# Performance work log

Measured on AMD Instinct MI355X. Metric: run time of the kernel, lower is better.

## Reference

```python
import jax, jax.numpy as jnp
import numpy as np

B, N, F, T, E, OUT = 16, 5000, 8, 12, 160000, 64


def setup_inputs() -> dict:
    key = jax.random.key(0)
    ks = jax.random.split(key, 20)
    d = {}
    d["x"] = jax.random.normal(ks[0], (B, N, F, T), dtype=jnp.float32)
    d["edge_index"] = jax.random.randint(ks[1], (2, E), 0, N, dtype=jnp.int32)
    def p(k, shape, scale=0.1):
        return jax.random.normal(k, shape, dtype=jnp.float32) * scale
    i = 2
    for g in ("z", "r", "h"):
        d[f"W{g}"] = p(ks[i], (F, OUT)); i += 1        # GCNConv weight
        d[f"b{g}"] = p(ks[i], (OUT,)); i += 1           # GCNConv bias
        d[f"L{g}"] = p(ks[i], (2 * OUT, OUT)); i += 1   # gate Linear weight
        d[f"lb{g}"] = p(ks[i], (OUT,)); i += 1          # gate Linear bias
    d["att"] = p(ks[i], (T,)); i += 1                   # A3TGCN attention logits
    d["fcW"] = p(ks[i], (OUT, T)); i += 1               # final Linear 64->periods
    d["fcb"] = p(ks[i], (T,))
    return d


def _gcn(xs, W, b, src, dst, norm, n_nodes):
    # xs: [M, N, F] -> D^{-1/2}(A+I)D^{-1/2} (xs W) + b
    support = xs @ W                                    # [M, N, OUT]
    msg = support[:, src, :] * norm[None, :, None]      # gather at source
    agg = jax.vmap(lambda m: jax.ops.segment_sum(m, dst, num_segments=n_nodes))(msg)
    return agg + b


def reference(x, edge_index, Wz, bz, Lz, lbz, Wr, br, Lr, lbr, Wh, bh, Lh, lbh, att, fcW, fcb):
    b_sz, n_nodes, _, periods = x.shape
    src, dst = edge_index[0], edge_index[1]
    loop = jnp.arange(n_nodes, dtype=src.dtype)
    src = jnp.concatenate([src, loop])                  # add self loops
    dst = jnp.concatenate([dst, loop])
    deg = jax.ops.segment_sum(jnp.ones(src.shape, jnp.float32), dst, num_segments=n_nodes)
    dinv = jnp.where(deg > 0, jax.lax.rsqrt(deg), 0.0)
    norm = dinv[src] * dinv[dst]                        # symmetric GCN normalization

    # In A3TGCN the hidden state is never carried across periods (stays zero),
    # so all periods are independent: fold T into the batch axis.
    xs = jnp.moveaxis(x, 3, 0).reshape(periods * b_sz, n_nodes, x.shape[2])
    H = jnp.zeros((periods * b_sz, n_nodes, Wz.shape[1]), x.dtype)

    Z = jax.nn.sigmoid(jnp.concatenate([_gcn(xs, Wz, bz, src, dst, norm, n_nodes), H], -1) @ Lz + lbz)
    R = jax.nn.sigmoid(jnp.concatenate([_gcn(xs, Wr, br, src, dst, norm, n_nodes), H], -1) @ Lr + lbr)
    Ht = jnp.tanh(jnp.concatenate([_gcn(xs, Wh, bh, src, dst, norm, n_nodes), H * R], -1) @ Lh + lbh)
    Hnew = Z * H + (1.0 - Z) * Ht                       # [T*B, N, 64]

    Hs = Hnew.reshape(periods, b_sz, n_nodes, -1)
    Hacc = jnp.einsum('t,tbnh->bnh', jax.nn.softmax(att), Hs)
    return Hacc @ fcW + fcb                             # [B, N, periods]
```

## Files before the change

kernel.cpp:

```cpp
#include <hip/hip_runtime.h>
#include <math.h>

#define BB 16
#define NN 5000
#define FF 8
#define TT 12
#define EE 160000
#define HH 64
#define EN (EE + NN)
#define XBSTRIDE 1920000
#define BSOFF    15360000


__global__ void k_count(const int* __restrict__ dst, int* __restrict__ deg) {
    int i = blockIdx.x * blockDim.x + threadIdx.x;
    if (i < EE) atomicAdd(&deg[dst[i]], 1);
}

__global__ __launch_bounds__(256) void k_scan_prep(
    const int* __restrict__ deg, int* __restrict__ offs, int* __restrict__ cursor,
    float* __restrict__ dinv,
    const float* __restrict__ Wz, const float* __restrict__ bz,
    const float* __restrict__ Lz, const float* __restrict__ lbz,
    const float* __restrict__ Wh, const float* __restrict__ bh,
    const float* __restrict__ Lh, const float* __restrict__ lbh,
    const float* __restrict__ att,
    float* __restrict__ G, float* __restrict__ C, float* __restrict__ sm) {
    int tid = threadIdx.x;
    if (blockIdx.x == 0) {
        __shared__ int s[256];
        int base = tid * 20;
        int cnt[20];
        int part = 0;
#pragma unroll
        for (int j = 0; j < 20; ++j) {
            int n = base + j;
            int c = (n < NN) ? deg[n] + 1 : 0;
            cnt[j] = c;
            part += c;
        }
        s[tid] = part;
        __syncthreads();
        for (int d = 1; d < 256; d <<= 1) {
            int v = (tid >= d) ? s[tid - d] : 0;
            __syncthreads();
            s[tid] += v;
            __syncthreads();
        }
        int run = s[tid] - part;
#pragma unroll
        for (int j = 0; j < 20; ++j) {
            int n = base + j;
            if (n < NN) {
                offs[n] = run;
                cursor[n] = run;
                dinv[n] = rsqrtf((float)cnt[j]);
                run += cnt[j];
            }
        }
        if (tid == 255) offs[NN] = s[255];
    } else {
        for (int idx = tid; idx < 1024; idx += 256) {
            int g = idx >> 9, rem = idx & 511, f = rem >> 6, o = rem & 63;
            const float* W = g ? Wh : Wz;
            const float* L = g ? Lh : Lz;
            float acc = 0.f;
            for (int k = 0; k < 64; ++k) acc += W[f * 64 + k] * L[k * 64 + o];
            G[idx] = acc;
        }
        for (int idx = tid; idx < 128; idx += 256) {
            int g = idx >> 6, o = idx & 63;
            const float* b = g ? bh : bz;
            const float* L = g ? Lh : Lz;
            const float* lb = g ? lbh : lbz;
            float acc = lb[o];
            for (int k = 0; k < 64; ++k) acc += b[k] * L[k * 64 + o];
            C[idx] = acc;
        }
        if (tid == 0) {
            float m = att[0];
            for (int t = 1; t < TT; ++t) m = fmaxf(m, att[t]);
            float e[TT], ss = 0.f;
            for (int t = 0; t < TT; ++t) { e[t] = __expf(att[t] - m); ss += e[t]; }
            for (int t = 0; t < TT; ++t) sm[t] = e[t] / ss;
        }
    }
}

__global__ void k_fill(const int* __restrict__ src, const int* __restrict__ dst,
                       int* cursor, const float* __restrict__ dinv,
                       int2* __restrict__ cedge) {
    int i = blockIdx.x * blockDim.x + threadIdx.x;
    if (i < EE) {
        int s = src[i], d = dst[i];
        int p = atomicAdd(&cursor[d], 1);
        cedge[p] = make_int2(s, __float_as_int(dinv[s] * dinv[d]));
    } else if (i < EN) {
        int n = i - EE;
        int p = atomicAdd(&cursor[n], 1);
        cedge[p] = make_int2(n, __float_as_int(dinv[n] * dinv[n]));
    } else if (i < EN + 8) {
        cedge[i] = make_int2(0, 0);
    }
}


#define EDGE(D)                                                         \
    {                                                                   \
        unsigned a_ = (unsigned)(D).x * 384u + voff;                    \
        float4 v_ = *(const float4*)(xbb + a_);                         \
        float w_ = __int_as_float((D).y);                               \
        acc.x += w_ * v_.x; acc.y += w_ * v_.y;                         \
        acc.z += w_ * v_.z; acc.w += w_ * v_.w;                         \
    }

__global__ __launch_bounds__(256) void k_fused(
    const float* __restrict__ x, const int* __restrict__ offs,
    const int2* __restrict__ cedge,
    const float* __restrict__ G, const float* __restrict__ C,
    const float* __restrict__ sm, const float* __restrict__ fcW,
    const float* __restrict__ fcb, float* __restrict__ out) {
    __shared__ __align__(16) float xals[4][2][96];
    __shared__ float hl[4][2][65];

    const int tid = threadIdx.x;
    const int wid = tid >> 6;
    const int lane = tid & 63;
    const int bp = blockIdx.x & 7;
    const int g = blockIdx.x >> 3;
    const int n = g * 4 + wid;

    int r0 = __builtin_amdgcn_readfirstlane(offs[n]);
    int r1 = __builtin_amdgcn_readfirstlane(offs[n + 1]);

    const char* xbb = (const char*)x + (size_t)bp * XBSTRIDE;

    if (lane < 48) {
        const unsigned voff = (unsigned)(lane / 24) * BSOFF + (unsigned)(lane % 24) * 16u;
        float4 acc = {0.f, 0.f, 0.f, 0.f};

        int k = r0;
        int2 p0 = cedge[k];
        int2 p1 = cedge[k + 1];
        int2 p2 = cedge[k + 2];
        int2 p3 = cedge[k + 3];
        while (k + 4 <= r1) {
            int2 d0 = p0, d1 = p1, d2 = p2, d3 = p3;
            k += 4;
            p0 = cedge[k];
            p1 = cedge[k + 1];
            p2 = cedge[k + 2];
            p3 = cedge[k + 3];
            EDGE(d0) EDGE(d1) EDGE(d2) EDGE(d3)
        }
        int rem = r1 - k;
        if (rem > 0) EDGE(p0)
        if (rem > 1) EDGE(p1)
        if (rem > 2) EDGE(p2)

        *(float4*)&xals[wid][lane / 24][(lane % 24) * 4] = acc;
    }
    __syncthreads();

    float gz[FF], gh[FF];
#pragma unroll
    for (int f = 0; f < FF; ++f) {
        gz[f] = G[f * 64 + lane];
        gh[f] = G[512 + f * 64 + lane];
    }
    float cz = C[lane], ch = C[64 + lane];
    float smv[TT];
#pragma unroll
    for (int t = 0; t < TT; ++t) smv[t] = sm[t];

#pragma unroll
    for (int bs = 0; bs < 2; ++bs) {
        float hacc = 0.f;
#pragma unroll
        for (int tq = 0; tq < 3; ++tq) {
            float4 xq[FF];
#pragma unroll
            for (int f = 0; f < FF; ++f)
                xq[f] = *(const float4*)&xals[wid][bs][f * TT + tq * 4];
#pragma unroll
            for (int tt = 0; tt < 4; ++tt) {
                float az = cz, ah = ch;
#pragma unroll
                for (int f = 0; f < FF; ++f) {
                    float v = ((const float*)&xq[f])[tt];
                    az += v * gz[f];
                    ah += v * gh[f];
                }
                float z = __builtin_amdgcn_rcpf(1.0f + __expf(-az));
                float th = 1.0f - 2.0f * __builtin_amdgcn_rcpf(__expf(2.0f * ah) + 1.0f);
                hacc += smv[tq * 4 + tt] * (1.0f - z) * th;
            }
        }
        hl[wid][bs][lane] = hacc;
    }
    __syncthreads();

    if (tid < 96) {
        int nw = tid / 24;
        int rem = tid % 24;
        int bs = rem / 12;
        int t = rem % 12;
        int nn2 = g * 4 + nw;
        int b = bp + bs * 8;
        float s = fcb[t];
#pragma unroll 16
        for (int o = 0; o < HH; ++o) s += hl[nw][bs][o] * fcW[o * TT + t];
        out[((size_t)b * NN + nn2) * TT + t] = s;
    }
}

extern "C" void kernel_launch(void* const* d_in, const int* in_sizes, int n_in,
                              void* d_out, int out_size, void* d_ws, size_t ws_size,
                              hipStream_t stream) {
    const float* x   = (const float*)d_in[0];
    const int*   ei  = (const int*)d_in[1];
    const float* Wz  = (const float*)d_in[2];
    const float* bz  = (const float*)d_in[3];
    const float* Lz  = (const float*)d_in[4];
    const float* lbz = (const float*)d_in[5];
    const float* Wh  = (const float*)d_in[10];
    const float* bh  = (const float*)d_in[11];
    const float* Lh  = (const float*)d_in[12];
    const float* lbh = (const float*)d_in[13];
    const float* att = (const float*)d_in[14];
    const float* fcW = (const float*)d_in[15];
    const float* fcb = (const float*)d_in[16];
    float* out = (float*)d_out;

    const int* src = ei;
    const int* dst = ei + EE;

    int2*  cedge  = (int2*)d_ws;
    int*   deg    = (int*)(cedge + EN + 8);
    int*   cursor = deg + NN;
    int*   offs   = cursor + NN;
    float* dinv   = (float*)(offs + NN + 1);
    float* G      = dinv + NN;
    float* C      = G + 1024;
    float* sm     = C + 128;

    hipMemsetAsync(deg, 0, NN * sizeof(int), stream);
    hipLaunchKernelGGL(k_count, dim3((EE + 255) / 256), dim3(256), 0, stream, dst, deg);
    hipLaunchKernelGGL(k_scan_prep, dim3(2), dim3(256), 0, stream,
                       deg, offs, cursor, dinv,
                       Wz, bz, Lz, lbz, Wh, bh, Lh, lbh, att, G, C, sm);
    hipLaunchKernelGGL(k_fill, dim3((EN + 8 + 255) / 256), dim3(256), 0, stream,
                       src, dst, cursor, dinv, cedge);
    hipLaunchKernelGGL(k_fused, dim3(1250 * 8), dim3(256), 0, stream,
                       x, offs, cedge, G, C, sm, fcW, fcb, out);
}
```

Baseline: 142.9 us.

## Pad CSR rows to multiples of 8 and vectorize gather, gates, and FC

Each node's CSR segment is padded to a multiple of 8 zero-weight entries, so the gather loop reads int4 edge pairs in blocks of 8 with no tail handling, at the cost of zeroing a larger workspace with memset. G, C and fcW are staged in LDS. Gate math uses exp2 with log2e folded into the precomputed weights, plus a combined sigmoid-tanh expression that needs a single reciprocal. The final linear layer writes two outputs per thread using packed float2 math. These changes cut the number of edge-load instructions, transcendental operations and global reads of the weights, while adding padding traffic and more LDS use.

```diff
diff --git a/kernel.cpp b/kernel.cpp
--- a/kernel.cpp
+++ b/kernel.cpp
@@ -1,15 +1,19 @@
 #include <hip/hip_runtime.h>
-#include <math.h>
-
-#define BB 16
+
 #define NN 5000
 #define FF 8
 #define TT 12
 #define EE 160000
 #define HH 64
 #define EN (EE + NN)
+#define CAP (EN + 7 * NN + 64)
 #define XBSTRIDE 1920000
 #define BSOFF    15360000
+
+typedef float f2  __attribute__((ext_vector_type(2)));
+typedef float f4v __attribute__((ext_vector_type(4)));
+
+#define LOG2E 1.44269504088896340736f
 
 
 __global__ void k_count(const int* __restrict__ dst, int* __restrict__ deg) {
@@ -30,14 +34,15 @@
     if (blockIdx.x == 0) {
         __shared__ int s[256];
         int base = tid * 20;
-        int cnt[20];
+        int pad[20], real[20];
         int part = 0;
 #pragma unroll
         for (int j = 0; j < 20; ++j) {
             int n = base + j;
             int c = (n < NN) ? deg[n] + 1 : 0;
-            cnt[j] = c;
-            part += c;
+            real[j] = c;
+            pad[j] = (c + 7) & ~7;
+            part += pad[j];
         }
         s[tid] = part;
         __syncthreads();
@@ -54,8 +59,8 @@
             if (n < NN) {
                 offs[n] = run;
                 cursor[n] = run;
-                dinv[n] = rsqrtf((float)cnt[j]);
-                run += cnt[j];
+                dinv[n] = rsqrtf((float)real[j]);
+                run += pad[j];
             }
         }
         if (tid == 255) offs[NN] = s[255];
@@ -66,7 +71,7 @@
             const float* L = g ? Lh : Lz;
             float acc = 0.f;
             for (int k = 0; k < 64; ++k) acc += W[f * 64 + k] * L[k * 64 + o];
-            G[idx] = acc;
+            G[idx] = acc * (g ? 2.0f * LOG2E : LOG2E);
         }
         for (int idx = tid; idx < 128; idx += 256) {
             int g = idx >> 6, o = idx & 63;
@@ -75,7 +80,7 @@
             const float* lb = g ? lbh : lbz;
             float acc = lb[o];
             for (int k = 0; k < 64; ++k) acc += b[k] * L[k * 64 + o];
-            C[idx] = acc;
+            C[idx] = acc * (g ? 2.0f * LOG2E : LOG2E);
         }
         if (tid == 0) {
             float m = att[0];
@@ -99,19 +104,18 @@
         int n = i - EE;
         int p = atomicAdd(&cursor[n], 1);
         cedge[p] = make_int2(n, __float_as_int(dinv[n] * dinv[n]));
-    } else if (i < EN + 8) {
-        cedge[i] = make_int2(0, 0);
-    }
-}
-
-
-#define EDGE(D)                                                         \
-    {                                                                   \
-        unsigned a_ = (unsigned)(D).x * 384u + voff;                    \
-        float4 v_ = *(const float4*)(xbb + a_);                         \
-        float w_ = __int_as_float((D).y);                               \
-        acc.x += w_ * v_.x; acc.y += w_ * v_.y;                         \
-        acc.z += w_ * v_.z; acc.w += w_ * v_.w;                         \
+    }
+}
+
+
+#define E2(Q)                                                     \
+    {                                                             \
+        unsigned a0_ = (unsigned)(Q).x * 384u + voff;             \
+        unsigned a1_ = (unsigned)(Q).z * 384u + voff;             \
+        f4v v0_ = *(const f4v*)(xbb + a0_);                       \
+        f4v v1_ = *(const f4v*)(xbb + a1_);                       \
+        acc += __int_as_float((Q).y) * v0_;                       \
+        acc += __int_as_float((Q).w) * v1_;                       \
     }
 
 __global__ __launch_bounds__(256) void k_fused(
@@ -121,7 +125,10 @@
     const float* __restrict__ sm, const float* __restrict__ fcW,
     const float* __restrict__ fcb, float* __restrict__ out) {
     __shared__ __align__(16) float xals[4][2][96];
-    __shared__ float hl[4][2][65];
+    __shared__ __align__(16) float hl[4][2][72];
+    __shared__ __align__(16) float fcw[768];
+    __shared__ __align__(16) float Glds[1024];
+    __shared__ __align__(16) float Clds[128];
 
     const int tid = threadIdx.x;
     const int wid = tid >> 6;
@@ -130,6 +137,10 @@
     const int g = blockIdx.x >> 3;
     const int n = g * 4 + wid;
 
+    ((f4v*)Glds)[tid] = ((const f4v*)G)[tid];
+    if (tid < 192) ((f4v*)fcw)[tid] = ((const f4v*)fcW)[tid];
+    if (tid < 32) ((f4v*)Clds)[tid] = ((const f4v*)C)[tid];
+
     int r0 = __builtin_amdgcn_readfirstlane(offs[n]);
     int r1 = __builtin_amdgcn_readfirstlane(offs[n + 1]);
 
@@ -137,38 +148,32 @@
 
     if (lane < 48) {
         const unsigned voff = (unsigned)(lane / 24) * BSOFF + (unsigned)(lane % 24) * 16u;
-        float4 acc = {0.f, 0.f, 0.f, 0.f};
-
-        int k = r0;
-        int2 p0 = cedge[k];
-        int2 p1 = cedge[k + 1];
-        int2 p2 = cedge[k + 2];
-        int2 p3 = cedge[k + 3];
-        while (k + 4 <= r1) {
-            int2 d0 = p0, d1 = p1, d2 = p2, d3 = p3;
-            k += 4;
-            p0 = cedge[k];
-            p1 = cedge[k + 1];
-            p2 = cedge[k + 2];
-            p3 = cedge[k + 3];
-            EDGE(d0) EDGE(d1) EDGE(d2) EDGE(d3)
-        }
-        int rem = r1 - k;
-        if (rem > 0) EDGE(p0)
-        if (rem > 1) EDGE(p1)
-        if (rem > 2) EDGE(p2)
-
-        *(float4*)&xals[wid][lane / 24][(lane % 24) * 4] = acc;
+        f4v acc = {0.f, 0.f, 0.f, 0.f};
+
+        const int4* ce = (const int4*)cedge;
+        int c = r0 >> 1;
+        const int c1 = r1 >> 1;
+        int4 A0 = ce[c], A1 = ce[c + 1], A2 = ce[c + 2], A3 = ce[c + 3];
+        int4 B0 = ce[c + 4], B1 = ce[c + 5], B2 = ce[c + 6], B3 = ce[c + 7];
+        while (true) {
+            int4 D0 = A0, D1 = A1, D2 = A2, D3 = A3;
+            A0 = B0; A1 = B1; A2 = B2; A3 = B3;
+            B0 = ce[c + 8]; B1 = ce[c + 9]; B2 = ce[c + 10]; B3 = ce[c + 11];
+            E2(D0) E2(D1) E2(D2) E2(D3)
+            c += 4;
+            if (c >= c1) break;
+        }
+        *(f4v*)&xals[wid][lane / 24][(lane % 24) * 4] = acc;
     }
     __syncthreads();
 
     float gz[FF], gh[FF];
 #pragma unroll
     for (int f = 0; f < FF; ++f) {
-        gz[f] = G[f * 64 + lane];
-        gh[f] = G[512 + f * 64 + lane];
-    }
-    float cz = C[lane], ch = C[64 + lane];
+        gz[f] = Glds[f * 64 + lane];
+        gh[f] = Glds[512 + f * 64 + lane];
+    }
+    float cz = Clds[lane], ch = Clds[64 + lane];
     float smv[TT];
 #pragma unroll
     for (int t = 0; t < TT; ++t) smv[t] = sm[t];
@@ -178,39 +183,57 @@
         float hacc = 0.f;
 #pragma unroll
         for (int tq = 0; tq < 3; ++tq) {
-            float4 xq[FF];
+            f4v xq[FF];
 #pragma unroll
             for (int f = 0; f < FF; ++f)
-                xq[f] = *(const float4*)&xals[wid][bs][f * TT + tq * 4];
-#pragma unroll
-            for (int tt = 0; tt < 4; ++tt) {
-                float az = cz, ah = ch;
+                xq[f] = *(const f4v*)&xals[wid][bs][f * TT + tq * 4];
+#pragma unroll
+            for (int half = 0; half < 2; ++half) {
+                f2 az = {cz, cz}, ah = {ch, ch};
 #pragma unroll
                 for (int f = 0; f < FF; ++f) {
-                    float v = ((const float*)&xq[f])[tt];
+                    f2 v = half ? xq[f].hi : xq[f].lo;
                     az += v * gz[f];
                     ah += v * gh[f];
                 }
-                float z = __builtin_amdgcn_rcpf(1.0f + __expf(-az));
-                float th = 1.0f - 2.0f * __builtin_amdgcn_rcpf(__expf(2.0f * ah) + 1.0f);
-                hacc += smv[tq * 4 + tt] * (1.0f - z) * th;
+#pragma unroll
+                for (int j = 0; j < 2; ++j) {
+                    float ea = exp2f(az[j]);
+                    float e2h = exp2f(ah[j]);
+                    float num = e2h - 1.0f;
+                    float den = (1.0f + ea) * (1.0f + e2h);
+                    hacc += smv[tq * 4 + half * 2 + j] * num * __builtin_amdgcn_rcpf(den);
+                }
             }
         }
         hl[wid][bs][lane] = hacc;
     }
     __syncthreads();
 
-    if (tid < 96) {
-        int nw = tid / 24;
-        int rem = tid % 24;
-        int bs = rem / 12;
-        int t = rem % 12;
+    if (tid < 48) {
+        int nw = tid / 12;
+        int rem = tid % 12;
+        int bs = rem / 6;
+        int tp = rem % 6;
+        f2 acc;
+        acc[0] = fcb[2 * tp];
+        acc[1] = fcb[2 * tp + 1];
+        const float* hrow = &hl[nw][bs][0];
+#pragma unroll
+        for (int o4 = 0; o4 < 16; ++o4) {
+            f4v h4 = *(const f4v*)&hrow[o4 * 4];
+            f2 w0 = *(const f2*)&fcw[(o4 * 4 + 0) * TT + 2 * tp];
+            f2 w1 = *(const f2*)&fcw[(o4 * 4 + 1) * TT + 2 * tp];
+            f2 w2 = *(const f2*)&fcw[(o4 * 4 + 2) * TT + 2 * tp];
+            f2 w3 = *(const f2*)&fcw[(o4 * 4 + 3) * TT + 2 * tp];
+            acc += h4[0] * w0;
+            acc += h4[1] * w1;
+            acc += h4[2] * w2;
+            acc += h4[3] * w3;
+        }
+        int b = bp + bs * 8;
         int nn2 = g * 4 + nw;
-        int b = bp + bs * 8;
-        float s = fcb[t];
-#pragma unroll 16
-        for (int o = 0; o < HH; ++o) s += hl[nw][bs][o] * fcW[o * TT + t];
-        out[((size_t)b * NN + nn2) * TT + t] = s;
+        *(f2*)&out[((size_t)b * NN + nn2) * TT + 2 * tp] = acc;
     }
 }
 
@@ -236,7 +259,7 @@
     const int* dst = ei + EE;
 
     int2*  cedge  = (int2*)d_ws;
-    int*   deg    = (int*)(cedge + EN + 8);
+    int*   deg    = (int*)(cedge + CAP);
     int*   cursor = deg + NN;
     int*   offs   = cursor + NN;
     float* dinv   = (float*)(offs + NN + 1);
@@ -244,12 +267,12 @@
     float* C      = G + 1024;
     float* sm     = C + 128;
 
-    hipMemsetAsync(deg, 0, NN * sizeof(int), stream);
+    (void)hipMemsetAsync(d_ws, 0, (size_t)CAP * 8 + (size_t)NN * 4, stream);
     hipLaunchKernelGGL(k_count, dim3((EE + 255) / 256), dim3(256), 0, stream, dst, deg);
     hipLaunchKernelGGL(k_scan_prep, dim3(2), dim3(256), 0, stream,
                        deg, offs, cursor, dinv,
                        Wz, bz, Lz, lbz, Wh, bh, Lh, lbh, att, G, C, sm);
-    hipLaunchKernelGGL(k_fill, dim3((EN + 8 + 255) / 256), dim3(256), 0, stream,
+    hipLaunchKernelGGL(k_fill, dim3((EN + 255) / 256), dim3(256), 0, stream,
                        src, dst, cursor, dinv, cedge);
     hipLaunchKernelGGL(k_fused, dim3(1250 * 8), dim3(256), 0, stream,
                        x, offs, cedge, G, C, sm, fcW, fcb, out);
```

Result: faster. 137.5 us (-3.8%).
